# Optimization experiments

Measured on AMD Instinct MI355X. Metric: run time of the kernel, lower is better.

Reference implementation:

```python
import jax, jax.numpy as jnp
import numpy as np

B, S, V, CTX, NC, D, NH, L, FF, MAXS = 8, 512, 32000, 8, 512, 256, 4, 4, 512, 512
PAD = 0  # ram_model.pad_token_id


def setup_inputs() -> dict:
    key = jax.random.key(0)
    ks = iter(jax.random.split(key, 64))
    def p(shape, s=0.02):
        return jax.random.normal(next(ks), shape, jnp.float32) * s
    inp = {}
    inp["token_ids"] = jax.random.randint(next(ks), (B, S), 0, V)
    inp["ram_table"] = p((V, NC), 0.1)          # frozen RAM per-cluster scores
    inp["proj_W"] = p((NC, D)); inp["proj_b"] = jnp.zeros((D,), jnp.float32)
    inp["pos_emb"] = p((MAXS, D))
    for pre in ("sa", "ca"):
        for nm in ("Wq", "Wk", "Wv", "Wo"):
            inp[f"{pre}_{nm}"] = p((L, D, D))
        for nm in ("bq", "bk", "bv", "bo"):
            inp[f"{pre}_{nm}"] = jnp.zeros((L, D), jnp.float32)
    for i in (1, 2, 3):
        inp[f"ln{i}_s"] = jnp.ones((L, D), jnp.float32)
        inp[f"ln{i}_b"] = jnp.zeros((L, D), jnp.float32)
    inp["ff_W1"] = p((L, D, FF)); inp["ff_b1"] = jnp.zeros((L, FF), jnp.float32)
    inp["ff_W2"] = p((L, FF, D)); inp["ff_b2"] = jnp.zeros((L, D), jnp.float32)
    inp["out_W"] = p((D, V)); inp["out_b"] = jnp.zeros((V,), jnp.float32)
    return inp


def _ln(x, s, b):
    m = x.mean(-1, keepdims=True)
    v = ((x - m) ** 2).mean(-1, keepdims=True)
    return (x - m) * jax.lax.rsqrt(v + 1e-5) * s + b


def _mha(q_in, k_in, v_in, Wq, bq, Wk, bk, Wv, bv, Wo, bo, mask):
    b, sq, d = q_in.shape
    hd = d // NH
    q = (q_in @ Wq + bq).reshape(b, sq, NH, hd)
    k = (k_in @ Wk + bk).reshape(b, -1, NH, hd)
    v = (v_in @ Wv + bv).reshape(b, -1, NH, hd)
    sc = jnp.einsum("bqhd,bkhd->bhqk", q, k) / np.sqrt(hd).astype(np.float32)
    if mask is not None:
        sc = jnp.where(mask, -1e9, sc)  # mask broadcast over [b, h]
    a = jax.nn.softmax(sc, axis=-1)
    o = jnp.einsum("bhqk,bkhd->bqhd", a, v).reshape(b, sq, d)
    return o @ Wo + bo


def _forward(token_ids, ram_table, proj_W, proj_b, pos_emb,
             sa_Wq, sa_bq, sa_Wk, sa_bk, sa_Wv, sa_bv, sa_Wo, sa_bo,
             ca_Wq, ca_bq, ca_Wk, ca_bk, ca_Wv, ca_bv, ca_Wo, ca_bo,
             ln1_s, ln1_b, ln2_s, ln2_b, ln3_s, ln3_b,
             ff_W1, ff_b1, ff_W2, ff_b2, out_W, out_b):
    b, s = token_ids.shape
    # Batched sliding context windows (replaces the per-position Python loop):
    # left-pad with PAD so window at pos covers [pos-CTX+1, pos].
    padded = jnp.concatenate(
        [jnp.full((b, CTX - 1), PAD, token_ids.dtype), token_ids], axis=1)
    idx = jnp.arange(s)[:, None] + jnp.arange(CTX)[None, :]  # [S, CTX]
    win = padded[:, idx]                                      # [B, S, CTX]
    # Frozen RAM feature extraction: per-cluster scores averaged over window.
    scores = ram_table[win].mean(axis=2)                      # [B, S, NC]
    x = scores @ proj_W + proj_b + pos_emb[:s]                # [B, S, D]
    mask = jnp.triu(jnp.ones((s, s), bool), 1)                # causal
    mem = jnp.zeros((b, 1, D), x.dtype)
    for l in range(L):
        h = _ln(x, ln1_s[l], ln1_b[l])
        x = x + _mha(h, h, h, sa_Wq[l], sa_bq[l], sa_Wk[l], sa_bk[l],
                     sa_Wv[l], sa_bv[l], sa_Wo[l], sa_bo[l], mask)
        h = _ln(x, ln2_s[l], ln2_b[l])
        x = x + _mha(h, mem, mem, ca_Wq[l], ca_bq[l], ca_Wk[l], ca_bk[l],
                     ca_Wv[l], ca_bv[l], ca_Wo[l], ca_bo[l], None)
        h = _ln(x, ln3_s[l], ln3_b[l])
        x = x + jax.nn.relu(h @ ff_W1[l] + ff_b1[l]) @ ff_W2[l] + ff_b2[l]
    return x @ out_W + out_b                                  # [B, S, V]


def reference(token_ids, ram_table, proj_W, proj_b, pos_emb,
              sa_Wq, sa_bq, sa_Wk, sa_bk, sa_Wv, sa_bv, sa_Wo, sa_bo,
              ca_Wq, ca_bq, ca_Wk, ca_bk, ca_Wv, ca_bv, ca_Wo, ca_bo,
              ln1_s, ln1_b, ln2_s, ln2_b, ln3_s, ln3_b,
              ff_W1, ff_b1, ff_W2, ff_b2, out_W, out_b):
    return _forward(token_ids, ram_table, proj_W, proj_b, pos_emb,
                    sa_Wq, sa_bq, sa_Wk, sa_bk, sa_Wv, sa_bv, sa_Wo, sa_bo,
                    ca_Wq, ca_bq, ca_Wk, ca_bk, ca_Wv, ca_bv, ca_Wo, ca_bo,
                    ln1_s, ln1_b, ln2_s, ln2_b, ln3_s, ln3_b,
                    ff_W1, ff_b1, ff_W2, ff_b2, out_W, out_b)
```

## Files before the change

### kernel.cpp

```cpp
#include <hip/hip_runtime.h>

#define B_   8
#define S_   512
#define V_   32000
#define CTX_ 8
#define NC_  512
#define D_   256
#define NH_  4
#define L_   4
#define FF_  512
#define HD_  64
#define BS_  4096

#define FG_F32   1
#define FG_BF16  2
#define FG_RELU  4
#define FG_POS   8
#define FG_NT    16
#define FG_QKV   32

typedef __attribute__((ext_vector_type(8))) short bf16x8;
typedef __attribute__((ext_vector_type(4))) float f32x4;

__device__ inline void gload16(const void* g, void* lds) {
    __builtin_amdgcn_global_load_lds(
        (const __attribute__((address_space(1))) void*)g,
        (__attribute__((address_space(3))) void*)lds, 16, 0, 0);
}

__device__ inline ushort f2b(float f) {
    union { float f; unsigned u; } v; v.f = f;
    unsigned u = v.u;
    unsigned r = u + 0x7fffu + ((u >> 16) & 1u);
    return (ushort)(r >> 16);
}

__global__ __launch_bounds__(256) void prologue_kernel(
    const int* __restrict__ tok, const float* __restrict__ ram,
    const float* __restrict__ proj_W, const float* __restrict__ Wq,
    const float* __restrict__ Wk, const float* __restrict__ Wv,
    const float* __restrict__ Wo, const float* __restrict__ W1,
    const float* __restrict__ W2, const float* __restrict__ outW,
    const float* __restrict__ ca_bv, const float* __restrict__ ca_Wo,
    const float* __restrict__ ca_bo, const float* __restrict__ bq,
    const float* __restrict__ bk, const float* __restrict__ bv,
    ushort* __restrict__ pjWb, ushort* __restrict__ WqkvB,
    ushort* __restrict__ WoB, ushort* __restrict__ ff1B,
    ushort* __restrict__ ff2B, ushort* __restrict__ Wb,
    float* __restrict__ cc, float* __restrict__ qkvb,
    ushort* __restrict__ scores)
{
    __shared__ float tile[32 * 33];
    int id = blockIdx.x;
    int t = threadIdx.x;
    if (id < 10176) {
        const float* src; ushort* dst; int K, N, lt;
        if (id < 128)       { src = proj_W; dst = pjWb; K = 512; N = 256; lt = id; }
        else if (id < 896)  { lt = id - 128; int z = lt >> 6; lt &= 63;
                              int which = z / L_, l = z % L_;
                              src = (which == 0 ? Wq : which == 1 ? Wk : Wv) + (size_t)l * 65536;
                              dst = WqkvB + ((size_t)l * 768 + which * 256) * 256;
                              K = 256; N = 256; }
        else if (id < 1152) { lt = id - 896; int l = lt >> 6; lt &= 63;
                              src = Wo + (size_t)l * 65536; dst = WoB + (size_t)l * 65536;
                              K = 256; N = 256; }
        else if (id < 1664) { lt = id - 1152; int l = lt >> 7; lt &= 127;
                              src = W1 + (size_t)l * 131072; dst = ff1B + (size_t)l * 131072;
                              K = 256; N = 512; }
        else if (id < 2176) { lt = id - 1664; int l = lt >> 7; lt &= 127;
                              src = W2 + (size_t)l * 131072; dst = ff2B + (size_t)l * 131072;
                              K = 512; N = 256; }
        else                { lt = id - 2176; src = outW; dst = Wb; K = 256; N = 32000; }
        int ntc = N >> 5;
        int n0 = (lt % ntc) * 32, k0 = (lt / ntc) * 32;
        int tx = t & 31, ty = t >> 5;
        for (int i = ty; i < 32; i += 8)
            tile[i * 33 + tx] = src[(size_t)(k0 + i) * N + n0 + tx];
        __syncthreads();
        for (int i = ty; i < 32; i += 8)
            dst[(size_t)(n0 + i) * K + k0 + tx] = f2b(tile[tx * 33 + i]);
    } else if (id < 10180) {
        int l = id - 10176;
        const float* w = ca_Wo + (size_t)l * D_ * D_;
        const float* b = ca_bv + l * D_;
        float acc = 0.f;
        for (int d = 0; d < D_; ++d) acc += b[d] * w[(size_t)d * D_ + t];
        cc[l * D_ + t] = acc + ca_bo[l * D_ + t];
        for (int u = t; u < 768; u += 256) {
            int which = u >> 8, c = u & 255;
            const float* src = which == 0 ? bq : which == 1 ? bk : bv;
            qkvb[l * 768 + u] = src[l * 256 + c];
        }
    } else {
        int bs = id - 10180;
        int b = bs >> 9, s = bs & 511;
        float a0 = 0.f, a1 = 0.f;
        #pragma unroll
        for (int c = 0; c < CTX_; ++c) {
            int pos = s + c - (CTX_ - 1);
            int tk = (pos < 0) ? 0 : tok[b * S_ + pos];
            const float* row = ram + (size_t)tk * NC_;
            a0 += row[t];
            a1 += row[t + 256];
        }
        scores[(size_t)bs * NC_ + t]       = f2b(a0 * 0.125f);
        scores[(size_t)bs * NC_ + t + 256] = f2b(a1 * 0.125f);
    }
}

template<int K, int FLAGS>
__global__ __launch_bounds__(256) void gemm_row(
    const ushort* __restrict__ A, const ushort* __restrict__ Bt,
    const float* __restrict__ bias, const float* __restrict__ extra,
    const float* __restrict__ resid, const float* __restrict__ pos,
    const float* __restrict__ lnS, const float* __restrict__ lnB,
    float* __restrict__ Xout, ushort* __restrict__ Hout)
{
    __shared__ ushort As[16 * 64];
    __shared__ ushort Bs[256 * 64];
    __shared__ float red[2][4][16];
    int mt = blockIdx.x;
    int row0 = mt * 16;
    int t = threadIdx.x, w = t >> 6, lane = t & 63;
    int srow = lane >> 3, slot = lane & 7;
    int gcol = (slot ^ srow) * 8;
    int sl = lane >> 4, lc = lane & 15;
    int rA = lane & 15;

    f32x4 acc[4] = {};

    #pragma unroll
    for (int k0 = 0; k0 < K; k0 += 64) {
        if (w < 2)
            gload16(A + (size_t)(row0 + w * 8 + srow) * K + k0 + gcol, As + w * 512);
        #pragma unroll
        for (int c = 0; c < 8; ++c) {
            int chunk = w * 8 + c;
            gload16(Bt + (size_t)(chunk * 8 + srow) * K + k0 + gcol, Bs + chunk * 512);
        }
        __syncthreads();
        #pragma unroll
        for (int kk = 0; kk < 2; ++kk) {
            bf16x8 a = *reinterpret_cast<const bf16x8*>(
                As + rA * 64 + (((sl + kk * 4) ^ (rA & 7)) * 8));
            #pragma unroll
            for (int n = 0; n < 4; ++n) {
                int rr = w * 64 + n * 16 + lc;
                rr = w * 64 + (lane & 15) + n * 16;
                bf16x8 b = *reinterpret_cast<const bf16x8*>(
                    Bs + rr * 64 + (((sl + kk * 4) ^ (rr & 7)) * 8));
                acc[n] = __builtin_amdgcn_mfma_f32_16x16x32_bf16(a, b, acc[n], 0, 0, 0);
            }
        }
        __syncthreads();
    }

    float v[4][4];
    float psum[4] = {}, psq[4] = {};
    #pragma unroll
    for (int n = 0; n < 4; ++n) {
        int col = w * 64 + n * 16 + lc;
        float bn = bias[col];
        float en = extra ? extra[col] : 0.f;
        #pragma unroll
        for (int r = 0; r < 4; ++r) {
            int row = row0 + sl * 4 + r;
            float x = acc[n][r] + bn;
            if constexpr (FLAGS & FG_POS) x += pos[(size_t)(row & 511) * D_ + col];
            x += en;
            if (resid) x += resid[(size_t)row * D_ + col];
            v[n][r] = x;
            psum[r] += x;
            psq[r] += x * x;
        }
    }
    #pragma unroll
    for (int r = 0; r < 4; ++r) {
        #pragma unroll
        for (int o = 8; o > 0; o >>= 1) {
            psum[r] += __shfl_xor(psum[r], o);
            psq[r]  += __shfl_xor(psq[r], o);
        }
    }
    if (lc == 0) {
        #pragma unroll
        for (int r = 0; r < 4; ++r) {
            red[0][w][sl * 4 + r] = psum[r];
            red[1][w][sl * 4 + r] = psq[r];
        }
    }
    __syncthreads();
    #pragma unroll
    for (int r = 0; r < 4; ++r) {
        int rl = sl * 4 + r;
        float s  = red[0][0][rl] + red[0][1][rl] + red[0][2][rl] + red[0][3][rl];
        float s2 = red[1][0][rl] + red[1][1][rl] + red[1][2][rl] + red[1][3][rl];
        float mean = s * (1.f / D_);
        float var = s2 * (1.f / D_) - mean * mean;
        float rstd = rsqrtf(var + 1e-5f);
        int row = row0 + rl;
        #pragma unroll
        for (int n = 0; n < 4; ++n) {
            int col = w * 64 + n * 16 + lc;
            float x = v[n][r];
            Xout[(size_t)row * D_ + col] = x;
            Hout[(size_t)row * D_ + col] =
                f2b((x - mean) * rstd * lnS[col] + lnB[col]);
        }
    }
}

template<int BM, int BN, int K, int TN, int FLAGS>
__global__ __launch_bounds__(256) void gemm_t(
    const ushort* __restrict__ A, const ushort* __restrict__ Bt,
    const float* __restrict__ bias, const float* __restrict__ extra,
    const float* __restrict__ resid, const float* __restrict__ pos,
    float* __restrict__ Cf, ushort* __restrict__ Cb)
{
    constexpr int WM = BM / 32;
    constexpr int WN = BN / 32;
    constexpr int MT = 4096 / BM;
    constexpr int NWG = MT * (TN / BN);
    __shared__ ushort smem[(BM + BN) * 64];
    ushort* As = smem;
    ushort* Bs = smem + BM * 64;
    int bid = blockIdx.x;
    int swz = bid;
    if constexpr ((NWG & 7) == 0) {
        constexpr int cpx = NWG >> 3;
        swz = (bid & 7) * cpx + (bid >> 3);
    }
    int mt = swz % MT, nt = swz / MT;
    int row0 = mt * BM, col0 = nt * BN;
    int t = threadIdx.x, w = t >> 6, lane = t & 63;
    int wr = w >> 1, wc = w & 1;
    int srow = lane >> 3, slot = lane & 7;
    int gcol = (slot ^ srow) * 8;

    f32x4 acc[WM][WN] = {};
    int sl = lane >> 4;
    int rA0 = wr * (BM / 2) + (lane & 15);
    int rB0 = wc * (BN / 2) + (lane & 15);

    #pragma unroll
    for (int k0 = 0; k0 < K; k0 += 64) {
        #pragma unroll
        for (int c = 0; c < BM / 32; ++c) {
            int chunk = w * (BM / 32) + c;
            gload16(A + (size_t)(row0 + chunk * 8 + srow) * K + k0 + gcol,
                    As + chunk * 512);
        }
        #pragma unroll
        for (int c = 0; c < BN / 32; ++c) {
            int chunk = w * (BN / 32) + c;
            gload16(Bt + (size_t)(col0 + chunk * 8 + srow) * K + k0 + gcol,
                    Bs + chunk * 512);
        }
        __syncthreads();
        #pragma unroll
        for (int kk = 0; kk < 2; ++kk) {
            bf16x8 a[WM], b[WN];
            #pragma unroll
            for (int m = 0; m < WM; ++m) {
                int rr = rA0 + m * 16;
                a[m] = *reinterpret_cast<const bf16x8*>(
                    As + rr * 64 + (((sl + kk * 4) ^ (rr & 7)) * 8));
            }
            #pragma unroll
            for (int n = 0; n < WN; ++n) {
                int rr = rB0 + n * 16;
                b[n] = *reinterpret_cast<const bf16x8*>(
                    Bs + rr * 64 + (((sl + kk * 4) ^ (rr & 7)) * 8));
            }
            #pragma unroll
            for (int m = 0; m < WM; ++m)
                #pragma unroll
                for (int n = 0; n < WN; ++n)
                    acc[m][n] = __builtin_amdgcn_mfma_f32_16x16x32_bf16(
                        a[m], b[n], acc[m][n], 0, 0, 0);
        }
        __syncthreads();
    }

    int lr = (lane >> 4) * 4;
    int lc = lane & 15;

    if constexpr (FLAGS & FG_NT) {
        float* Ct = reinterpret_cast<float*>(smem);
        #pragma unroll
        for (int p = 0; p < 2; ++p) {
            __syncthreads();
            if (wr == p) {
                #pragma unroll
                for (int n = 0; n < WN; ++n) {
                    int colL = wc * (BN / 2) + n * 16 + lc;
                    float bn = bias[col0 + colL];
                    #pragma unroll
                    for (int m = 0; m < WM; ++m)
                        #pragma unroll
                        for (int r = 0; r < 4; ++r)
                            Ct[(m * 16 + lr + r) * BN + colL] = acc[m][n][r] + bn;
                }
            }
            __syncthreads();
            constexpr int NV4 = (BM / 2) * (BN / 4);
            #pragma unroll
            for (int j = 0; j < NV4 / 256; ++j) {
                int idx = t + j * 256;
                int rl = idx / (BN / 4);
                int c4 = idx % (BN / 4);
                f32x4 v4 = reinterpret_cast<const f32x4*>(Ct)[idx];
                __builtin_nontemporal_store(v4,
                    reinterpret_cast<f32x4*>(
                        &Cf[(size_t)(row0 + p * (BM / 2) + rl) * TN + col0 + c4 * 4]));
            }
        }
        return;
    }

    #pragma unroll
    for (int n = 0; n < WN; ++n) {
        int col = col0 + wc * (BN / 2) + n * 16 + lc;
        float bn = bias ? bias[col] : 0.f;
        float en = extra ? extra[col] : 0.f;
        #pragma unroll
        for (int m = 0; m < WM; ++m) {
            int rbase = row0 + wr * (BM / 2) + m * 16 + lr;
            #pragma unroll
            for (int r = 0; r < 4; ++r) {
                int row = rbase + r;
                float v = acc[m][n][r] + bn;
                if constexpr (FLAGS & FG_QKV) {
                    int which = col >> 8;
                    int c2 = col & 255;
                    int hh = c2 >> 6, dd = c2 & 63;
                    int bb = row >> 9, ss = row & 511;
                    if (which == 0) {
                        Cb[((((size_t)bb * NH_ + hh) * S_ + ss) << 6) + dd] =
                            f2b(v * 0.125f);
                    } else if (which == 1) {
                        (Cb + 1048576)[((((size_t)bb * NH_ + hh) * S_ + ss) << 6) + dd] =
                            f2b(v);
                    } else {
                        (Cb + 2097152)[((((size_t)bb * NH_ + hh) * HD_ + dd) << 9) + ss] =
                            f2b(v);
                    }
                } else {
                    if constexpr (FLAGS & FG_POS) v += pos[(size_t)(row & 511) * TN + col];
                    if (extra) v += en;
                    if (resid) v += resid[(size_t)row * TN + col];
                    if constexpr (FLAGS & FG_RELU) v = fmaxf(v, 0.f);
                    if constexpr (FLAGS & FG_BF16)
                        Cb[(size_t)row * TN + col] = f2b(v);
                    if constexpr (FLAGS & FG_F32)
                        Cf[(size_t)row * TN + col] = v;
                }
            }
        }
    }
}

__global__ __launch_bounds__(256) void attn_kernel(
    const ushort* __restrict__ q, const ushort* __restrict__ k,
    const ushort* __restrict__ vT, ushort* __restrict__ pv)
{
    int qt = blockIdx.x, bh = blockIdx.y;
    __shared__ ushort smem[20480];
    ushort* Ps = smem + 16384;
    int t = threadIdx.x, w = t >> 6, lane = t & 63;
    int srow = lane >> 3, slot = lane & 7;
    int gcol = (slot ^ srow) * 8;
    int sl = lane >> 4, lc = lane & 15;

    const ushort* Qp = q + ((size_t)bh * S_ + qt * 64) * HD_;
    const ushort* Kp = k + (size_t)bh * S_ * HD_;
    const ushort* Vp = vT + (size_t)bh * HD_ * S_;

    int qrow = w * 16 + lc;
    bf16x8 qf0 = *reinterpret_cast<const bf16x8*>(Qp + qrow * 64 + sl * 8);
    bf16x8 qf1 = *reinterpret_cast<const bf16x8*>(Qp + qrow * 64 + sl * 8 + 32);

    f32x4 o[4] = {};
    float m_r[4], l_r[4];
    #pragma unroll
    for (int r = 0; r < 4; ++r) { m_r[r] = -1e30f; l_r[r] = 0.f; }
    int row_abs = qt * 64 + w * 16 + sl * 4;

    {
        ushort* Ks = smem;
        ushort* Vs = smem + 4096;
        #pragma unroll
        for (int c = 0; c < 2; ++c) {
            int chunk = w * 2 + c;
            gload16(Kp + (size_t)(chunk * 8 + srow) * 64 + gcol, Ks + chunk * 512);
            gload16(Vp + (size_t)(chunk * 8 + srow) * 512 + gcol, Vs + chunk * 512);
        }
    }

    for (int kt = 0; kt <= qt; ++kt) {
        int cur = kt & 1;
        ushort* Ks = smem + cur * 8192;
        ushort* Vs = smem + cur * 8192 + 4096;
        __syncthreads();
        if (kt < qt) {
            ushort* Kn = smem + (cur ^ 1) * 8192;
            ushort* Vn = Kn + 4096;
            #pragma unroll
            for (int c = 0; c < 2; ++c) {
                int chunk = w * 2 + c;
                gload16(Kp + (size_t)((kt + 1) * 64 + chunk * 8 + srow) * 64 + gcol,
                        Kn + chunk * 512);
                gload16(Vp + (size_t)(chunk * 8 + srow) * 512 + (kt + 1) * 64 + gcol,
                        Vn + chunk * 512);
            }
        }

        f32x4 sa[4] = {};
        #pragma unroll
        for (int n = 0; n < 4; ++n) {
            int rB = n * 16 + lc;
            bf16x8 b0 = *reinterpret_cast<const bf16x8*>(
                Ks + rB * 64 + ((sl ^ (rB & 7)) * 8));
            bf16x8 b1 = *reinterpret_cast<const bf16x8*>(
                Ks + rB * 64 + (((sl + 4) ^ (rB & 7)) * 8));
            sa[n] = __builtin_amdgcn_mfma_f32_16x16x32_bf16(qf0, b0, sa[n], 0, 0, 0);
            sa[n] = __builtin_amdgcn_mfma_f32_16x16x32_bf16(qf1, b1, sa[n], 0, 0, 0);
        }
        if (kt == qt) {
            #pragma unroll
            for (int n = 0; n < 4; ++n) {
                int col = kt * 64 + n * 16 + lc;
                #pragma unroll
                for (int r = 0; r < 4; ++r)
                    if (col > row_abs + r) sa[n][r] = -1e30f;
            }
        }
        float psum[4];
        #pragma unroll
        for (int r = 0; r < 4; ++r) {
            float vm = fmaxf(fmaxf(sa[0][r], sa[1][r]), fmaxf(sa[2][r], sa[3][r]));
            vm = fmaxf(vm, __shfl_xor(vm, 1));
            vm = fmaxf(vm, __shfl_xor(vm, 2));
            vm = fmaxf(vm, __shfl_xor(vm, 4));
            vm = fmaxf(vm, __shfl_xor(vm, 8));
            float mn = fmaxf(m_r[r], vm);
            float scl = __expf(m_r[r] - mn);
            m_r[r] = mn;
            l_r[r] *= scl;
            #pragma unroll
            for (int n = 0; n < 4; ++n) o[n][r] *= scl;
            psum[r] = 0.f;
        }
        ushort* Pw = Ps + w * 1024;
        #pragma unroll
        for (int n = 0; n < 4; ++n) {
            #pragma unroll
            for (int r = 0; r < 4; ++r) {
                float p = __expf(sa[n][r] - m_r[r]);
                psum[r] += p;
                int prow = sl * 4 + r;
                int pcol = n * 16 + lc;
                int pslot = pcol >> 3;
                Pw[prow * 64 + ((pslot ^ (prow & 7)) * 8) + (pcol & 7)] = f2b(p);
            }
        }
        #pragma unroll
        for (int r = 0; r < 4; ++r) {
            float s = psum[r];
            s += __shfl_xor(s, 1);
            s += __shfl_xor(s, 2);
            s += __shfl_xor(s, 4);
            s += __shfl_xor(s, 8);
            l_r[r] += s;
        }
        int arow = lc;
        bf16x8 pa0 = *reinterpret_cast<const bf16x8*>(
            Pw + arow * 64 + ((sl ^ (arow & 7)) * 8));
        bf16x8 pa1 = *reinterpret_cast<const bf16x8*>(
            Pw + arow * 64 + (((sl + 4) ^ (arow & 7)) * 8));
        #pragma unroll
        for (int n = 0; n < 4; ++n) {
            int rB = n * 16 + lc;
            bf16x8 v0 = *reinterpret_cast<const bf16x8*>(
                Vs + rB * 64 + ((sl ^ (rB & 7)) * 8));
            bf16x8 v1 = *reinterpret_cast<const bf16x8*>(
                Vs + rB * 64 + (((sl + 4) ^ (rB & 7)) * 8));
            o[n] = __builtin_amdgcn_mfma_f32_16x16x32_bf16(pa0, v0, o[n], 0, 0, 0);
            o[n] = __builtin_amdgcn_mfma_f32_16x16x32_bf16(pa1, v1, o[n], 0, 0, 0);
        }
    }

    int bb = bh >> 2, hh = bh & 3;
    #pragma unroll
    for (int r = 0; r < 4; ++r) {
        float inv = 1.f / l_r[r];
        int ss = qt * 64 + w * 16 + sl * 4 + r;
        #pragma unroll
        for (int n = 0; n < 4; ++n) {
            int dd = n * 16 + lc;
            pv[((size_t)bb * S_ + ss) * D_ + hh * HD_ + dd] = f2b(o[n][r] * inv);
        }
    }
}

extern "C" void kernel_launch(void* const* d_in, const int* in_sizes, int n_in,
                              void* d_out, int out_size, void* d_ws, size_t ws_size,
                              hipStream_t stream)
{
    const int*   tok     = (const int*)  d_in[0];
    const float* ram     = (const float*)d_in[1];
    const float* proj_W  = (const float*)d_in[2];
    const float* proj_b  = (const float*)d_in[3];
    const float* pos_emb = (const float*)d_in[4];
    const float* sa_Wq   = (const float*)d_in[5];
    const float* sa_Wk   = (const float*)d_in[6];
    const float* sa_Wv   = (const float*)d_in[7];
    const float* sa_Wo   = (const float*)d_in[8];
    const float* sa_bq   = (const float*)d_in[9];
    const float* sa_bk   = (const float*)d_in[10];
    const float* sa_bv   = (const float*)d_in[11];
    const float* sa_bo   = (const float*)d_in[12];
    const float* ca_Wo   = (const float*)d_in[16];
    const float* ca_bv   = (const float*)d_in[19];
    const float* ca_bo   = (const float*)d_in[20];
    const float* ln1_s   = (const float*)d_in[21];
    const float* ln1_b   = (const float*)d_in[22];
    const float* ln3_s   = (const float*)d_in[25];
    const float* ln3_b   = (const float*)d_in[26];
    const float* ff_W1   = (const float*)d_in[27];
    const float* ff_b1   = (const float*)d_in[28];
    const float* ff_W2   = (const float*)d_in[29];
    const float* ff_b2   = (const float*)d_in[30];
    const float* out_W   = (const float*)d_in[31];
    const float* out_b   = (const float*)d_in[32];

    float* out = (float*)d_out;
    float* ws  = (float*)d_ws;

    float*  x   = ws;
    float*  cc  = ws + (size_t)BS_ * D_;
    ushort* xb  = (ushort*)(cc + L_ * D_);
    ushort* Wb  = xb + (size_t)BS_ * D_;

    ushort* sc_b  = (ushort*)out;
    ushort* h_b   = sc_b + 2097152;
    ushort* qkv3  = h_b + 1048576;
    ushort* pv_b  = qkv3 + 3145728;
    ushort* ffh_b = pv_b + 1048576;
    ushort* pjWb  = ffh_b + 2097152;
    ushort* WqkvB = pjWb + 131072;
    ushort* WoB   = WqkvB + 786432;
    ushort* ff1B  = WoB + 262144;
    ushort* ff2B  = ff1B + 524288;
    float*  qkvb  = (float*)(ff2B + 524288);
    ushort* qb_b  = qkv3;
    ushort* kb_b  = qkv3 + 1048576;
    ushort* vT_b  = qkv3 + 2097152;

    prologue_kernel<<<14276, 256, 0, stream>>>(
        tok, ram, proj_W, sa_Wq, sa_Wk, sa_Wv, sa_Wo, ff_W1, ff_W2, out_W,
        ca_bv, ca_Wo, ca_bo, sa_bq, sa_bk, sa_bv,
        pjWb, WqkvB, WoB, ff1B, ff2B, Wb, cc, qkvb, sc_b);

    gemm_row<512, FG_POS><<<256, 256, 0, stream>>>(
        sc_b, pjWb, proj_b, nullptr, nullptr, pos_emb,
        ln1_s, ln1_b, x, h_b);

    for (int l = 0; l < L_; ++l) {
        gemm_t<64, 64, 256, 768, FG_QKV><<<768, 256, 0, stream>>>(
            h_b, WqkvB + (size_t)l * 196608, qkvb + l * 768,
            nullptr, nullptr, nullptr, nullptr, qkv3);
        attn_kernel<<<dim3(8, 32), 256, 0, stream>>>(qb_b, kb_b, vT_b, pv_b);
        gemm_row<256, 0><<<256, 256, 0, stream>>>(
            pv_b, WoB + (size_t)l * 65536, sa_bo + l * D_,
            cc + l * D_, x, nullptr, ln3_s + l * D_, ln3_b + l * D_, x, h_b);
        gemm_t<64, 64, 256, 512, FG_BF16 | FG_RELU><<<512, 256, 0, stream>>>(
            h_b, ff1B + (size_t)l * 131072, ff_b1 + l * FF_,
            nullptr, nullptr, nullptr, nullptr, ffh_b);
        if (l < L_ - 1) {
            gemm_row<512, 0><<<256, 256, 0, stream>>>(
                ffh_b, ff2B + (size_t)l * 131072, ff_b2 + l * D_,
                nullptr, x, nullptr, ln1_s + (l + 1) * D_, ln1_b + (l + 1) * D_,
                x, h_b);
        } else {
            gemm_t<64, 64, 512, 256, FG_BF16><<<256, 256, 0, stream>>>(
                ffh_b, ff2B + (size_t)l * 131072, ff_b2 + l * D_,
                nullptr, x, nullptr, nullptr, xb);
        }
    }

    gemm_t<128, 128, 256, 32000, FG_F32 | FG_NT><<<8000, 256, 0, stream>>>(
        xb, Wb, out_b, nullptr, nullptr, nullptr, out, nullptr);
}
```

Measured before the change: 389.2 us.

## Fuse FFN up-projection, ReLU, down-projection and LayerNorm into one kernel

Replaces the separate FF1 GEMM (writing the bf16 hidden activation to global memory) and the FF2 row-GEMM with a single kernel per 16-row block. The kernel computes each 64-wide slice of the hidden layer in LDS, applies bias and ReLU, and immediately accumulates it into the output, then applies residual and LayerNorm (or writes bf16 for the last layer). This removes the intermediate global round-trip and one launch per layer. In exchange each block streams all of W1 and W2 with only 256 blocks, so per-block work and weight reloads grow and the K-loop is serialized with several syncs per chunk.

```diff
diff --git a/kernel.cpp b/kernel.cpp
--- a/kernel.cpp
+++ b/kernel.cpp
@@ -145,8 +145,7 @@
                 As + rA * 64 + (((sl + kk * 4) ^ (rA & 7)) * 8));
             #pragma unroll
             for (int n = 0; n < 4; ++n) {
-                int rr = w * 64 + n * 16 + lc;
-                rr = w * 64 + (lane & 15) + n * 16;
+                int rr = w * 64 + (lane & 15) + n * 16;
                 bf16x8 b = *reinterpret_cast<const bf16x8*>(
                     Bs + rr * 64 + (((sl + kk * 4) ^ (rr & 7)) * 8));
                 acc[n] = __builtin_amdgcn_mfma_f32_16x16x32_bf16(a, b, acc[n], 0, 0, 0);
@@ -173,6 +172,156 @@
             psum[r] += x;
             psq[r] += x * x;
         }
+    }
+    #pragma unroll
+    for (int r = 0; r < 4; ++r) {
+        #pragma unroll
+        for (int o = 8; o > 0; o >>= 1) {
+            psum[r] += __shfl_xor(psum[r], o);
+            psq[r]  += __shfl_xor(psq[r], o);
+        }
+    }
+    if (lc == 0) {
+        #pragma unroll
+        for (int r = 0; r < 4; ++r) {
+            red[0][w][sl * 4 + r] = psum[r];
+            red[1][w][sl * 4 + r] = psq[r];
+        }
+    }
+    __syncthreads();
+    #pragma unroll
+    for (int r = 0; r < 4; ++r) {
+        int rl = sl * 4 + r;
+        float s  = red[0][0][rl] + red[0][1][rl] + red[0][2][rl] + red[0][3][rl];
+        float s2 = red[1][0][rl] + red[1][1][rl] + red[1][2][rl] + red[1][3][rl];
+        float mean = s * (1.f / D_);
+        float var = s2 * (1.f / D_) - mean * mean;
+        float rstd = rsqrtf(var + 1e-5f);
+        int row = row0 + rl;
+        #pragma unroll
+        for (int n = 0; n < 4; ++n) {
+            int col = w * 64 + n * 16 + lc;
+            float x = v[n][r];
+            Xout[(size_t)row * D_ + col] = x;
+            Hout[(size_t)row * D_ + col] =
+                f2b((x - mean) * rstd * lnS[col] + lnB[col]);
+        }
+    }
+}
+
+template<bool LAST>
+__global__ __launch_bounds__(256) void ff_fused_kernel(
+    const ushort* __restrict__ H, const ushort* __restrict__ W1t,
+    const ushort* __restrict__ W2t, const float* __restrict__ b1,
+    const float* __restrict__ b2, const float* __restrict__ xin,
+    const float* __restrict__ lnS, const float* __restrict__ lnB,
+    float* __restrict__ Xout, ushort* __restrict__ Hout,
+    ushort* __restrict__ XBout)
+{
+    __shared__ ushort As[16 * 256];
+    __shared__ ushort Bs1[64 * 256];
+    __shared__ ushort Bs2[256 * 64];
+    __shared__ ushort As2[16 * 64];
+    __shared__ float red[2][4][16];
+    int row0 = blockIdx.x * 16;
+    int t = threadIdx.x, w = t >> 6, lane = t & 63;
+    int srow = lane >> 3, slot = lane & 7;
+    int gcol = (slot ^ srow) * 8;
+    int sl = lane >> 4, lc = lane & 15;
+    int rA = lane & 15;
+
+    #pragma unroll
+    for (int c = 0; c < 2; ++c) {
+        int chunk = w * 2 + c;
+        int ks = chunk >> 1, rbit = chunk & 1;
+        gload16(H + (size_t)(row0 + rbit * 8 + srow) * 256 + ks * 64 + gcol,
+                As + chunk * 512);
+    }
+
+    f32x4 xacc[4] = {};
+
+    for (int c8 = 0; c8 < 8; ++c8) {
+        int f0 = c8 * 64;
+        #pragma unroll
+        for (int c = 0; c < 8; ++c) {
+            int chunk = w * 8 + c;
+            int ks = chunk >> 3, rg = chunk & 7;
+            gload16(W1t + (size_t)(f0 + rg * 8 + srow) * 256 + ks * 64 + gcol,
+                    Bs1 + chunk * 512);
+        }
+        #pragma unroll
+        for (int c = 0; c < 8; ++c) {
+            int chunk = w * 8 + c;
+            gload16(W2t + (size_t)(chunk * 8 + srow) * 512 + f0 + gcol,
+                    Bs2 + chunk * 512);
+        }
+        __syncthreads();
+
+        f32x4 a2 = {};
+        #pragma unroll
+        for (int ks = 0; ks < 4; ++ks) {
+            #pragma unroll
+            for (int kk = 0; kk < 2; ++kk) {
+                bf16x8 a = *reinterpret_cast<const bf16x8*>(
+                    As + ks * 1024 + rA * 64 + (((sl + kk * 4) ^ (rA & 7)) * 8));
+                int rB = w * 16 + rA;
+                bf16x8 b = *reinterpret_cast<const bf16x8*>(
+                    Bs1 + ks * 4096 + rB * 64 + (((sl + kk * 4) ^ (rB & 7)) * 8));
+                a2 = __builtin_amdgcn_mfma_f32_16x16x32_bf16(a, b, a2, 0, 0, 0);
+            }
+        }
+        {
+            float bn = b1[f0 + w * 16 + lc];
+            #pragma unroll
+            for (int r = 0; r < 4; ++r) {
+                float p = fmaxf(a2[r] + bn, 0.f);
+                int prow = sl * 4 + r;
+                int pcol = w * 16 + lc;
+                As2[prow * 64 + (((pcol >> 3) ^ (prow & 7)) * 8) + (pcol & 7)] = f2b(p);
+            }
+        }
+        __syncthreads();
+        #pragma unroll
+        for (int kk = 0; kk < 2; ++kk) {
+            bf16x8 a = *reinterpret_cast<const bf16x8*>(
+                As2 + rA * 64 + (((sl + kk * 4) ^ (rA & 7)) * 8));
+            #pragma unroll
+            for (int n = 0; n < 4; ++n) {
+                int rB = w * 64 + n * 16 + rA;
+                bf16x8 b = *reinterpret_cast<const bf16x8*>(
+                    Bs2 + rB * 64 + (((sl + kk * 4) ^ (rB & 7)) * 8));
+                xacc[n] = __builtin_amdgcn_mfma_f32_16x16x32_bf16(a, b, xacc[n], 0, 0, 0);
+            }
+        }
+        __syncthreads();
+    }
+
+    float v[4][4];
+    float psum[4] = {}, psq[4] = {};
+    #pragma unroll
+    for (int n = 0; n < 4; ++n) {
+        int col = w * 64 + n * 16 + lc;
+        float bn = b2[col];
+        #pragma unroll
+        for (int r = 0; r < 4; ++r) {
+            int row = row0 + sl * 4 + r;
+            float x = xacc[n][r] + bn + xin[(size_t)row * D_ + col];
+            v[n][r] = x;
+            psum[r] += x;
+            psq[r] += x * x;
+        }
+    }
+    if constexpr (LAST) {
+        #pragma unroll
+        for (int n = 0; n < 4; ++n) {
+            int col = w * 64 + n * 16 + lc;
+            #pragma unroll
+            for (int r = 0; r < 4; ++r) {
+                int row = row0 + sl * 4 + r;
+                XBout[(size_t)row * D_ + col] = f2b(v[n][r]);
+            }
+        }
+        return;
     }
     #pragma unroll
     for (int r = 0; r < 4; ++r) {
@@ -546,8 +695,7 @@
     ushort* h_b   = sc_b + 2097152;
     ushort* qkv3  = h_b + 1048576;
     ushort* pv_b  = qkv3 + 3145728;
-    ushort* ffh_b = pv_b + 1048576;
-    ushort* pjWb  = ffh_b + 2097152;
+    ushort* pjWb  = pv_b + 1048576;
     ushort* WqkvB = pjWb + 131072;
     ushort* WoB   = WqkvB + 786432;
     ushort* ff1B  = WoB + 262144;
@@ -574,18 +722,16 @@
         gemm_row<256, 0><<<256, 256, 0, stream>>>(
             pv_b, WoB + (size_t)l * 65536, sa_bo + l * D_,
             cc + l * D_, x, nullptr, ln3_s + l * D_, ln3_b + l * D_, x, h_b);
-        gemm_t<64, 64, 256, 512, FG_BF16 | FG_RELU><<<512, 256, 0, stream>>>(
-            h_b, ff1B + (size_t)l * 131072, ff_b1 + l * FF_,
-            nullptr, nullptr, nullptr, nullptr, ffh_b);
         if (l < L_ - 1) {
-            gemm_row<512, 0><<<256, 256, 0, stream>>>(
-                ffh_b, ff2B + (size_t)l * 131072, ff_b2 + l * D_,
-                nullptr, x, nullptr, ln1_s + (l + 1) * D_, ln1_b + (l + 1) * D_,
-                x, h_b);
+            ff_fused_kernel<false><<<256, 256, 0, stream>>>(
+                h_b, ff1B + (size_t)l * 131072, ff2B + (size_t)l * 131072,
+                ff_b1 + l * FF_, ff_b2 + l * D_, x,
+                ln1_s + (l + 1) * D_, ln1_b + (l + 1) * D_, x, h_b, nullptr);
         } else {
-            gemm_t<64, 64, 512, 256, FG_BF16><<<256, 256, 0, stream>>>(
-                ffh_b, ff2B + (size_t)l * 131072, ff_b2 + l * D_,
-                nullptr, x, nullptr, nullptr, xb);
+            ff_fused_kernel<true><<<256, 256, 0, stream>>>(
+                h_b, ff1B + (size_t)l * 131072, ff2B + (size_t)l * 131072,
+                ff_b1 + l * FF_, ff_b2 + l * D_, x,
+                nullptr, nullptr, nullptr, nullptr, xb);
         }
     }
 
```

Measured after the change: 380.1 us. 2.4% less time.
